# Kernel optimization log

Measured on AMD Instinct MI355X. Metric: run time of the kernel, lower is better.

The kernel has to match this reference:

```python
import jax, jax.numpy as jnp
import numpy as np

N_FFT = 1024
HOP = 256
CACHE = N_FFT - 1  # causal left padding
EPS = 1e-12
BATCH = 16
SAMPLES = HOP * 2048


def _make_weight():
    # DFT basis modulated by a periodic Hann window (torch.hann_window default).
    n = np.arange(N_FFT, dtype=np.float32)
    k = np.arange(N_FFT // 2 + 1, dtype=np.float32)[:, None]
    ang = (-2.0 * np.pi / N_FFT) * k * n[None, :]
    win = 0.5 * (1.0 - np.cos(2.0 * np.pi * n / N_FFT))
    w = np.concatenate([np.cos(ang), np.sin(ang)], axis=0) * win  # [2*(N//2+1), N_FFT]
    return jnp.asarray(w, dtype=jnp.float32)[:, None, :]  # [O, I=1, K]


def setup_inputs() -> dict:
    key = jax.random.key(0)
    x = jax.random.normal(key, (BATCH, SAMPLES), dtype=jnp.float32)
    return {"x": x, "weight": _make_weight()}


def reference(x, weight):
    if x.ndim == 2:
        x = x[:, None, :]  # [B, 1, T]
    # causal constant (zero) padding on the left
    x = jnp.pad(x, ((0, 0), (0, 0), (CACHE, 0)))
    # strided conv against the fixed DFT basis: [B, 2*(N//2+1), L]
    y = jax.lax.conv_general_dilated(
        x, weight, window_strides=(HOP,), padding='VALID',
        dimension_numbers=('NCH', 'OIH', 'NCH'))
    B, C, T = y.shape
    y = y.reshape(B, 2, C // 2, T)  # real/imag split
    mag = jnp.sqrt(jnp.clip(jnp.sum(y * y, axis=1), EPS, None))  # [B, N//2+1, L]
    return mag
```

## Files before the change

### kernel.cpp

```cpp
#include <hip/hip_runtime.h>
#include <stdint.h>

#define SAMPLES   524288
#define BATCH     16
#define T_FRAMES  2048
#define K_FFT     1024
#define HOPSZ     256
#define CACHEPAD  1023
#define NCH       513
#define XROW      525312

typedef __bf16          bf16x8 __attribute__((ext_vector_type(8)));
typedef float           f32x4  __attribute__((ext_vector_type(4)));
typedef unsigned short  u16x8  __attribute__((ext_vector_type(8)));

__device__ __forceinline__ unsigned short f2bf(float f) {
    union { float f; unsigned u; } v; v.f = f;
    unsigned r = v.u + 0x7fffu + ((v.u >> 16) & 1u);
    return (unsigned short)(r >> 16);
}

__global__ void prep(const float* __restrict__ x, const float* __restrict__ wsrc,
                     unsigned short* __restrict__ Xb, unsigned short* __restrict__ Wb) {
    const int bid = blockIdx.x;
    const int tid = threadIdx.x;
    if (bid < 512) {
        int gid = bid * 256 + tid;
        int m   = gid >> 7;
        int kc  = (gid & 127) << 3;
        int q = m >> 5, h = (m >> 4) & 1, r = m & 15;
        int bin  = q * 16 + r;
        int srow = (h == 0) ? bin : (bin == 0 ? 512 : NCH + bin);
        const float* s = wsrc + (long long)srow * K_FFT + kc;
        f32x4 a = *(const f32x4*)s;
        f32x4 c = *(const f32x4*)(s + 4);
        union { u16x8 v; unsigned short e[8]; } o;
        o.e[0]=f2bf(a[0]); o.e[1]=f2bf(a[1]); o.e[2]=f2bf(a[2]); o.e[3]=f2bf(a[3]);
        o.e[4]=f2bf(c[0]); o.e[5]=f2bf(c[1]); o.e[6]=f2bf(c[2]); o.e[7]=f2bf(c[3]);
        *(u16x8*)(Wb + (long long)m * K_FFT + kc) = o.v;
    } else {
        int id  = bid - 512;
        int bat = id >> 8;
        int bx  = id & 255;
        unsigned short* xbo = Xb + (long long)bat * XROW;
        if (bx == 0) {
            for (int j = tid; j < CACHEPAD; j += 256) xbo[j] = 0;
            if (tid == 0) xbo[XROW - 1] = 0;
        }
        int i0 = (bx * 256 + tid) * 8;
        const float* xb = x + (long long)bat * SAMPLES;
        f32x4 a = *(const f32x4*)&xb[i0];
        f32x4 c = *(const f32x4*)&xb[i0 + 4];
        unsigned short* dst = xbo + CACHEPAD + i0;
        dst[0]=f2bf(a[0]); dst[1]=f2bf(a[1]); dst[2]=f2bf(a[2]); dst[3]=f2bf(a[3]);
        dst[4]=f2bf(c[0]); dst[5]=f2bf(c[1]); dst[6]=f2bf(c[2]); dst[7]=f2bf(c[3]);
    }
}

__device__ __forceinline__ void gll16(const unsigned short* g, unsigned short* s) {
    __builtin_amdgcn_global_load_lds(
        (const __attribute__((address_space(1))) void*)g,
        (__attribute__((address_space(3))) void*)s,
        16, 0, 0);
}

__global__ __launch_bounds__(256, 3)
void stft_gemm(const unsigned short* __restrict__ Xb,
               const unsigned short* __restrict__ Wb,
               float* __restrict__ out) {
    __shared__ unsigned short Ws[128 * 64];
    __shared__ unsigned short Fs[128 * 64];

    const int id  = blockIdx.x;
    const int xcd = id & 7;
    const int idx = id >> 3;
    const int nt  = idx >> 5;
    const int ft  = (xcd << 5) | (idx & 31);

    const int tid = threadIdx.x;
    const int l   = tid & 63;
    const int w   = tid >> 6;
    const int ln  = l & 15;
    const int qd  = l >> 4;

    const int b  = ft >> 4;
    const int t0 = (ft & 15) * 128;

    const unsigned short* xbase = Xb + (long long)b * XROW;

    const int srow   = l >> 3;
    const int schunk = l & 7;

    const unsigned short* fsrc[4];
    const unsigned short* wsrc[4];
    unsigned short* fdst[4];
    unsigned short* wdst[4];
    #pragma unroll
    for (int c = 0; c < 4; ++c) {
        int r = w * 32 + c * 8 + srow;
        int gchunk = schunk ^ (r & 7);
        fsrc[c] = xbase + (t0 + r) * HOPSZ + gchunk * 8;
        wsrc[c] = Wb + ((long long)(nt * 128 + r)) * K_FFT + gchunk * 8;
        fdst[c] = Fs + (w * 32 + c * 8) * 64;
        wdst[c] = Ws + (w * 32 + c * 8) * 64;
    }

    const int wave_m = w & 1;
    const int wave_n = w >> 1;

    f32x4 acc[4][4];
    #pragma unroll
    for (int i = 0; i < 4; ++i)
        #pragma unroll
        for (int j = 0; j < 4; ++j)
            acc[i][j] = (f32x4){0.f, 0.f, 0.f, 0.f};

    int a_off[4][2], b_off[4][2];
    #pragma unroll
    for (int i = 0; i < 4; ++i)
        #pragma unroll
        for (int k2 = 0; k2 < 2; ++k2) {
            int ck = ((k2 * 4 + qd) ^ (ln & 7)) * 8;
            a_off[i][k2] = (wave_m * 64 + i * 16 + ln) * 64 + ck;
            b_off[i][k2] = (wave_n * 64 + i * 16 + ln) * 64 + ck;
        }

    for (int kk = 0; kk < K_FFT; kk += 64) {
        #pragma unroll
        for (int c = 0; c < 4; ++c) gll16(fsrc[c] + kk, fdst[c]);
        #pragma unroll
        for (int c = 0; c < 4; ++c) gll16(wsrc[c] + kk, wdst[c]);
        __syncthreads();

        #pragma unroll
        for (int k2 = 0; k2 < 2; ++k2) {
            bf16x8 av[4], bv[4];
            #pragma unroll
            for (int i = 0; i < 4; ++i) av[i] = *(const bf16x8*)&Ws[a_off[i][k2]];
            #pragma unroll
            for (int j = 0; j < 4; ++j) bv[j] = *(const bf16x8*)&Fs[b_off[j][k2]];
            #pragma unroll
            for (int i = 0; i < 4; ++i)
                #pragma unroll
                for (int j = 0; j < 4; ++j)
                    acc[i][j] = __builtin_amdgcn_mfma_f32_16x16x32_bf16(av[i], bv[j], acc[i][j], 0, 0, 0);
        }
        __syncthreads();
    }

    float* outb = out + (long long)b * (NCH * T_FRAMES);
    #pragma unroll
    for (int p = 0; p < 2; ++p) {
        #pragma unroll
        for (int j = 0; j < 4; ++j) {
            const int t = t0 + wave_n * 64 + j * 16 + ln;
            #pragma unroll
            for (int r = 0; r < 4; ++r) {
                float re  = acc[2 * p][j][r];
                float im  = acc[2 * p + 1][j][r];
                int bin = (nt * 4 + wave_m * 2 + p) * 16 + qd * 4 + r;
                if (bin == 0) {
                    outb[t] = sqrtf(fmaxf(re * re, 1e-12f));
                    outb[(long long)512 * T_FRAMES + t] = sqrtf(fmaxf(im * im, 1e-12f));
                } else {
                    outb[(long long)bin * T_FRAMES + t] =
                        sqrtf(fmaxf(re * re + im * im, 1e-12f));
                }
            }
        }
    }
}

extern "C" void kernel_launch(void* const* d_in, const int* in_sizes, int n_in,
                              void* d_out, int out_size, void* d_ws, size_t ws_size,
                              hipStream_t stream) {
    const float* x  = (const float*)d_in[0];
    const float* wt = (const float*)d_in[1];
    float* out = (float*)d_out;

    unsigned short* Xb = (unsigned short*)d_ws;
    unsigned short* Wb = (unsigned short*)((char*)d_ws + (size_t)33554432);

    prep<<<4608, 256, 0, stream>>>(x, wt, Xb, Wb);
    stft_gemm<<<2048, 256, 0, stream>>>(Xb, Wb, out);
}
```

Measured before the change: 154.1 us.

## Switch GEMM to 32x32x16 MFMA tiles and vectorize padded bf16 input stores

The inner product now uses 32x32x16 bf16 MFMA instructions with 2x2 accumulator tiles per wave instead of 4x4 tiles of 16x16x32. This cuts the number of MFMA issues and LDS fragment loads per k-step, and the epilogue is remapped so real and imaginary parts come from one accumulator. The prep kernel also shifts the bf16 input by one element so each thread writes an aligned 16-byte vector instead of eight scalar stores, patching the boundary element separately. The risk is correctness in the new accumulator-to-bin mapping and in the shifted padding layout.

```diff
diff --git a/kernel.cpp b/kernel.cpp
--- a/kernel.cpp
+++ b/kernel.cpp
@@ -12,6 +12,7 @@
 
 typedef __bf16          bf16x8 __attribute__((ext_vector_type(8)));
 typedef float           f32x4  __attribute__((ext_vector_type(4)));
+typedef float           f32x16 __attribute__((ext_vector_type(16)));
 typedef unsigned short  u16x8  __attribute__((ext_vector_type(8)));
 
 __device__ __forceinline__ unsigned short f2bf(float f) {
@@ -45,15 +46,18 @@
         unsigned short* xbo = Xb + (long long)bat * XROW;
         if (bx == 0) {
             for (int j = tid; j < CACHEPAD; j += 256) xbo[j] = 0;
-            if (tid == 0) xbo[XROW - 1] = 0;
         }
         int i0 = (bx * 256 + tid) * 8;
         const float* xb = x + (long long)bat * SAMPLES;
         f32x4 a = *(const f32x4*)&xb[i0];
         f32x4 c = *(const f32x4*)&xb[i0 + 4];
-        unsigned short* dst = xbo + CACHEPAD + i0;
-        dst[0]=f2bf(a[0]); dst[1]=f2bf(a[1]); dst[2]=f2bf(a[2]); dst[3]=f2bf(a[3]);
-        dst[4]=f2bf(c[0]); dst[5]=f2bf(c[1]); dst[6]=f2bf(c[2]); dst[7]=f2bf(c[3]);
+        float e = (i0 + 8 < SAMPLES) ? xb[i0 + 8] : 0.f;
+        union { u16x8 v; unsigned short s[8]; } o;
+        o.s[0]=f2bf(a[1]); o.s[1]=f2bf(a[2]); o.s[2]=f2bf(a[3]);
+        o.s[3]=f2bf(c[0]); o.s[4]=f2bf(c[1]); o.s[5]=f2bf(c[2]); o.s[6]=f2bf(c[3]);
+        o.s[7]=f2bf(e);
+        *(u16x8*)(xbo + 1024 + i0) = o.v;
+        if (i0 == 0) xbo[CACHEPAD] = f2bf(a[0]);
     }
 }
 
@@ -80,8 +84,6 @@
     const int tid = threadIdx.x;
     const int l   = tid & 63;
     const int w   = tid >> 6;
-    const int ln  = l & 15;
-    const int qd  = l >> 4;
 
     const int b  = ft >> 4;
     const int t0 = (ft & 15) * 128;
@@ -107,22 +109,25 @@
 
     const int wave_m = w & 1;
     const int wave_n = w >> 1;
+    const int l31 = l & 31;
+    const int lh  = l >> 5;
 
-    f32x4 acc[4][4];
+    f32x16 acc[2][2];
     #pragma unroll
-    for (int i = 0; i < 4; ++i)
+    for (int i = 0; i < 2; ++i)
         #pragma unroll
-        for (int j = 0; j < 4; ++j)
-            acc[i][j] = (f32x4){0.f, 0.f, 0.f, 0.f};
+        for (int j = 0; j < 2; ++j)
+            acc[i][j] = (f32x16){0.f,0.f,0.f,0.f,0.f,0.f,0.f,0.f,
+                                 0.f,0.f,0.f,0.f,0.f,0.f,0.f,0.f};
 
-    int a_off[4][2], b_off[4][2];
+    int a_off[2][4], b_off[2][4];
     #pragma unroll
-    for (int i = 0; i < 4; ++i)
+    for (int i = 0; i < 2; ++i)
         #pragma unroll
-        for (int k2 = 0; k2 < 2; ++k2) {
-            int ck = ((k2 * 4 + qd) ^ (ln & 7)) * 8;
-            a_off[i][k2] = (wave_m * 64 + i * 16 + ln) * 64 + ck;
-            b_off[i][k2] = (wave_n * 64 + i * 16 + ln) * 64 + ck;
+        for (int s = 0; s < 4; ++s) {
+            int ck = (((s * 2 + lh) ^ (l & 7))) * 8;
+            a_off[i][s] = (wave_m * 64 + i * 32 + l31) * 64 + ck;
+            b_off[i][s] = (wave_n * 64 + i * 32 + l31) * 64 + ck;
         }
 
     for (int kk = 0; kk < K_FFT; kk += 64) {
@@ -133,32 +138,32 @@
         __syncthreads();
 
         #pragma unroll
-        for (int k2 = 0; k2 < 2; ++k2) {
-            bf16x8 av[4], bv[4];
-            #pragma unroll
-            for (int i = 0; i < 4; ++i) av[i] = *(const bf16x8*)&Ws[a_off[i][k2]];
-            #pragma unroll
-            for (int j = 0; j < 4; ++j) bv[j] = *(const bf16x8*)&Fs[b_off[j][k2]];
-            #pragma unroll
-            for (int i = 0; i < 4; ++i)
-                #pragma unroll
-                for (int j = 0; j < 4; ++j)
-                    acc[i][j] = __builtin_amdgcn_mfma_f32_16x16x32_bf16(av[i], bv[j], acc[i][j], 0, 0, 0);
+        for (int s = 0; s < 4; ++s) {
+            bf16x8 a0 = *(const bf16x8*)&Ws[a_off[0][s]];
+            bf16x8 a1 = *(const bf16x8*)&Ws[a_off[1][s]];
+            bf16x8 b0 = *(const bf16x8*)&Fs[b_off[0][s]];
+            bf16x8 b1 = *(const bf16x8*)&Fs[b_off[1][s]];
+            acc[0][0] = __builtin_amdgcn_mfma_f32_32x32x16_bf16(a0, b0, acc[0][0], 0, 0, 0);
+            acc[0][1] = __builtin_amdgcn_mfma_f32_32x32x16_bf16(a0, b1, acc[0][1], 0, 0, 0);
+            acc[1][0] = __builtin_amdgcn_mfma_f32_32x32x16_bf16(a1, b0, acc[1][0], 0, 0, 0);
+            acc[1][1] = __builtin_amdgcn_mfma_f32_32x32x16_bf16(a1, b1, acc[1][1], 0, 0, 0);
         }
         __syncthreads();
     }
 
     float* outb = out + (long long)b * (NCH * T_FRAMES);
     #pragma unroll
-    for (int p = 0; p < 2; ++p) {
+    for (int i = 0; i < 2; ++i) {
+        const int group = nt * 4 + wave_m * 2 + i;
         #pragma unroll
-        for (int j = 0; j < 4; ++j) {
-            const int t = t0 + wave_n * 64 + j * 16 + ln;
+        for (int j = 0; j < 2; ++j) {
+            const int t = t0 + wave_n * 64 + j * 32 + l31;
             #pragma unroll
-            for (int r = 0; r < 4; ++r) {
-                float re  = acc[2 * p][j][r];
-                float im  = acc[2 * p + 1][j][r];
-                int bin = (nt * 4 + wave_m * 2 + p) * 16 + qd * 4 + r;
+            for (int r = 0; r < 8; ++r) {
+                const int mloc = (r & 3) + 8 * (r >> 2) + 4 * lh;
+                float re = acc[i][j][r];
+                float im = acc[i][j][r + 8];
+                int bin = group * 16 + mloc;
                 if (bin == 0) {
                     outb[t] = sqrtf(fmaxf(re * re, 1e-12f));
                     outb[(long long)512 * T_FRAMES + t] = sqrtf(fmaxf(im * im, 1e-12f));
```

Result: slower. 162.4 us (+5.4%).

## Exploit DFT symmetry to halve GEMM reduction via sum/difference frames

Applied to the files above, without the earlier changes.

Rewrites the STFT GEMM to use cosine/sine symmetry of the DFT basis. Each frame is folded into sum and difference halves (x[n]+x[N-n], x[n]-x[N-n]), so the real part uses only the sum frames and the imaginary part only the difference frames, over half the reduction length (512 instead of 1024). The prep kernel now materialises these folded frames explicitly, which is about twice the original signal footprint, and the work is split into two batch halves to bound workspace size. The intent is to halve MFMA work at the cost of a heavier preprocessing pass, more workspace traffic and four launches instead of two.

```diff
diff --git a/kernel.cpp b/kernel.cpp
--- a/kernel.cpp
+++ b/kernel.cpp
@@ -4,11 +4,14 @@
 #define SAMPLES   524288
 #define BATCH     16
 #define T_FRAMES  2048
-#define K_FFT     1024
 #define HOPSZ     256
-#define CACHEPAD  1023
 #define NCH       513
-#define XROW      525312
+#define KF        512
+#define MF        1152
+#define HALF_FR   16384
+
+#define SB_OFF    1183744
+#define DB_OFF    17960960
 
 typedef __bf16          bf16x8 __attribute__((ext_vector_type(8)));
 typedef float           f32x4  __attribute__((ext_vector_type(4)));
@@ -21,40 +24,67 @@
 }
 
 __global__ void prep(const float* __restrict__ x, const float* __restrict__ wsrc,
-                     unsigned short* __restrict__ Xb, unsigned short* __restrict__ Wb) {
-    const int bid = blockIdx.x;
+                     unsigned short* __restrict__ Wf,
+                     unsigned short* __restrict__ Sb,
+                     unsigned short* __restrict__ Db, int half) {
+    int bid = blockIdx.x;
     const int tid = threadIdx.x;
-    if (bid < 512) {
-        int gid = bid * 256 + tid;
-        int m   = gid >> 7;
-        int kc  = (gid & 127) << 3;
-        int q = m >> 5, h = (m >> 4) & 1, r = m & 15;
-        int bin  = q * 16 + r;
-        int srow = (h == 0) ? bin : (bin == 0 ? 512 : NCH + bin);
-        const float* s = wsrc + (long long)srow * K_FFT + kc;
-        f32x4 a = *(const f32x4*)s;
-        f32x4 c = *(const f32x4*)(s + 4);
-        union { u16x8 v; unsigned short e[8]; } o;
-        o.e[0]=f2bf(a[0]); o.e[1]=f2bf(a[1]); o.e[2]=f2bf(a[2]); o.e[3]=f2bf(a[3]);
-        o.e[4]=f2bf(c[0]); o.e[5]=f2bf(c[1]); o.e[6]=f2bf(c[2]); o.e[7]=f2bf(c[3]);
-        *(u16x8*)(Wb + (long long)m * K_FFT + kc) = o.v;
+    if (half == 0) {
+        if (bid < 288) {
+            int gid = bid * 256 + tid;
+            int m   = gid >> 6;
+            int n0  = (gid & 63) << 3;
+            int g = m >> 5, h = (m >> 4) & 1, r = m & 15;
+            int bin = g * 16 + r;
+            bool valid = h ? (bin >= 1 && bin <= 511) : (bin <= 512);
+            const float* ws = wsrc + (long long)(h ? NCH + bin : bin) * 1024;
+            union { u16x8 v; unsigned short e[8]; } o;
+            #pragma unroll
+            for (int e = 0; e < 8; ++e) {
+                int n = n0 + e;
+                float v = 0.f;
+                if (valid) v = (n < 511) ? ws[n + 1] : 0.5f * ws[512];
+                o.e[e] = f2bf(v);
+            }
+            *(u16x8*)(Wf + (long long)m * KF + n0) = o.v;
+            return;
+        }
+        bid -= 288;
+    }
+    const int fr = tid >> 6;
+    const int n0 = (tid & 63) << 3;
+    const long long f = (long long)bid * 4 + fr;
+    const int bat = half * 8 + (int)(f >> 11);
+    const int t   = (int)(f & 2047);
+    const float* xb = x + (long long)bat * SAMPLES;
+    float fwd[8], rev[8];
+    if (t >= 4) {
+        const f32x4* pf = (const f32x4*)(xb + (t * 256 + n0 - 1024));
+        f32x4 A = pf[0], B = pf[1], C = pf[2];
+        fwd[0]=A[2]; fwd[1]=A[3]; fwd[2]=B[0]; fwd[3]=B[1];
+        fwd[4]=B[2]; fwd[5]=B[3]; fwd[6]=C[0]; fwd[7]=C[1];
+        const f32x4* pr = (const f32x4*)(xb + (t * 256 - n0 - 8));
+        f32x4 D = pr[0], E = pr[1], F = pr[2];
+        rev[0]=F[0]; rev[1]=E[3]; rev[2]=E[2]; rev[3]=E[1];
+        rev[4]=E[0]; rev[5]=D[3]; rev[6]=D[2]; rev[7]=D[1];
     } else {
-        int id  = bid - 512;
-        int bat = id >> 8;
-        int bx  = id & 255;
-        unsigned short* xbo = Xb + (long long)bat * XROW;
-        if (bx == 0) {
-            for (int j = tid; j < CACHEPAD; j += 256) xbo[j] = 0;
-            if (tid == 0) xbo[XROW - 1] = 0;
-        }
-        int i0 = (bx * 256 + tid) * 8;
-        const float* xb = x + (long long)bat * SAMPLES;
-        f32x4 a = *(const f32x4*)&xb[i0];
-        f32x4 c = *(const f32x4*)&xb[i0 + 4];
-        unsigned short* dst = xbo + CACHEPAD + i0;
-        dst[0]=f2bf(a[0]); dst[1]=f2bf(a[1]); dst[2]=f2bf(a[2]); dst[3]=f2bf(a[3]);
-        dst[4]=f2bf(c[0]); dst[5]=f2bf(c[1]); dst[6]=f2bf(c[2]); dst[7]=f2bf(c[3]);
-    }
+        #pragma unroll
+        for (int e = 0; e < 8; ++e) {
+            int n  = n0 + e;
+            int pf = t * 256 + n + 1 - 1023;
+            int pr = t * 256 - n;
+            fwd[e] = (pf >= 0) ? xb[pf] : 0.f;
+            rev[e] = (pr >= 0) ? xb[pr] : 0.f;
+        }
+    }
+    union { u16x8 v; unsigned short e[8]; } so, dof;
+    #pragma unroll
+    for (int e = 0; e < 8; ++e) {
+        so.e[e]  = f2bf(fwd[e] + rev[e]);
+        dof.e[e] = f2bf(fwd[e] - rev[e]);
+    }
+    *(u16x8*)(Sb + f * KF + n0) = so.v;
+    *(u16x8*)(Db + f * KF + n0) = dof.v;
 }
 
 __device__ __forceinline__ void gll16(const unsigned short* g, unsigned short* s) {
@@ -65,17 +95,22 @@
 }
 
 __global__ __launch_bounds__(256, 3)
-void stft_gemm(const unsigned short* __restrict__ Xb,
-               const unsigned short* __restrict__ Wb,
-               float* __restrict__ out) {
+void stft_gemm(const unsigned short* __restrict__ Sb,
+               const unsigned short* __restrict__ Db,
+               const unsigned short* __restrict__ Wf,
+               float* __restrict__ out, int half) {
     __shared__ unsigned short Ws[128 * 64];
-    __shared__ unsigned short Fs[128 * 64];
+    __shared__ unsigned short Ss[128 * 64];
+    __shared__ unsigned short Ds[128 * 64];
 
     const int id  = blockIdx.x;
     const int xcd = id & 7;
     const int idx = id >> 3;
-    const int nt  = idx >> 5;
-    const int ft  = (xcd << 5) | (idx & 31);
+    const int nt  = idx >> 4;
+    const int ft  = (xcd << 4) | (idx & 15);
+    const int bh  = ft >> 4;
+    const int t0  = (ft & 15) * 128;
+    const long long fl0 = (long long)bh * 2048 + t0;
 
     const int tid = threadIdx.x;
     const int l   = tid & 63;
@@ -83,26 +118,25 @@
     const int ln  = l & 15;
     const int qd  = l >> 4;
 
-    const int b  = ft >> 4;
-    const int t0 = (ft & 15) * 128;
-
-    const unsigned short* xbase = Xb + (long long)b * XROW;
-
     const int srow   = l >> 3;
     const int schunk = l & 7;
 
-    const unsigned short* fsrc[4];
-    const unsigned short* wsrc[4];
-    unsigned short* fdst[4];
-    unsigned short* wdst[4];
+    const unsigned short* asrc[4];
+    const unsigned short* ssrc[4];
+    const unsigned short* dsrc[4];
+    unsigned short* adst[4];
+    unsigned short* sdst[4];
+    unsigned short* ddst[4];
     #pragma unroll
     for (int c = 0; c < 4; ++c) {
         int r = w * 32 + c * 8 + srow;
         int gchunk = schunk ^ (r & 7);
-        fsrc[c] = xbase + (t0 + r) * HOPSZ + gchunk * 8;
-        wsrc[c] = Wb + ((long long)(nt * 128 + r)) * K_FFT + gchunk * 8;
-        fdst[c] = Fs + (w * 32 + c * 8) * 64;
-        wdst[c] = Ws + (w * 32 + c * 8) * 64;
+        asrc[c] = Wf + (long long)(nt * 128 + r) * KF + gchunk * 8;
+        ssrc[c] = Sb + (fl0 + r) * KF + gchunk * 8;
+        dsrc[c] = Db + (fl0 + r) * KF + gchunk * 8;
+        adst[c] = Ws + (w * 32 + c * 8) * 64;
+        sdst[c] = Ss + (w * 32 + c * 8) * 64;
+        ddst[c] = Ds + (w * 32 + c * 8) * 64;
     }
 
     const int wave_m = w & 1;
@@ -125,29 +159,36 @@
             b_off[i][k2] = (wave_n * 64 + i * 16 + ln) * 64 + ck;
         }
 
-    for (int kk = 0; kk < K_FFT; kk += 64) {
-        #pragma unroll
-        for (int c = 0; c < 4; ++c) gll16(fsrc[c] + kk, fdst[c]);
-        #pragma unroll
-        for (int c = 0; c < 4; ++c) gll16(wsrc[c] + kk, wdst[c]);
+    for (int kk = 0; kk < KF; kk += 64) {
+        #pragma unroll
+        for (int c = 0; c < 4; ++c) gll16(asrc[c] + kk, adst[c]);
+        #pragma unroll
+        for (int c = 0; c < 4; ++c) gll16(ssrc[c] + kk, sdst[c]);
+        #pragma unroll
+        for (int c = 0; c < 4; ++c) gll16(dsrc[c] + kk, ddst[c]);
         __syncthreads();
 
         #pragma unroll
         for (int k2 = 0; k2 < 2; ++k2) {
-            bf16x8 av[4], bv[4];
+            bf16x8 av[4], bs[4], bd[4];
             #pragma unroll
             for (int i = 0; i < 4; ++i) av[i] = *(const bf16x8*)&Ws[a_off[i][k2]];
             #pragma unroll
-            for (int j = 0; j < 4; ++j) bv[j] = *(const bf16x8*)&Fs[b_off[j][k2]];
-            #pragma unroll
-            for (int i = 0; i < 4; ++i)
-                #pragma unroll
-                for (int j = 0; j < 4; ++j)
-                    acc[i][j] = __builtin_amdgcn_mfma_f32_16x16x32_bf16(av[i], bv[j], acc[i][j], 0, 0, 0);
+            for (int j = 0; j < 4; ++j) bs[j] = *(const bf16x8*)&Ss[b_off[j][k2]];
+            #pragma unroll
+            for (int j = 0; j < 4; ++j) bd[j] = *(const bf16x8*)&Ds[b_off[j][k2]];
+            #pragma unroll
+            for (int j = 0; j < 4; ++j) {
+                acc[0][j] = __builtin_amdgcn_mfma_f32_16x16x32_bf16(av[0], bs[j], acc[0][j], 0, 0, 0);
+                acc[1][j] = __builtin_amdgcn_mfma_f32_16x16x32_bf16(av[1], bd[j], acc[1][j], 0, 0, 0);
+                acc[2][j] = __builtin_amdgcn_mfma_f32_16x16x32_bf16(av[2], bs[j], acc[2][j], 0, 0, 0);
+                acc[3][j] = __builtin_amdgcn_mfma_f32_16x16x32_bf16(av[3], bd[j], acc[3][j], 0, 0, 0);
+            }
         }
         __syncthreads();
     }
 
+    const int b = half * 8 + bh;
     float* outb = out + (long long)b * (NCH * T_FRAMES);
     #pragma unroll
     for (int p = 0; p < 2; ++p) {
@@ -159,13 +200,9 @@
                 float re  = acc[2 * p][j][r];
                 float im  = acc[2 * p + 1][j][r];
                 int bin = (nt * 4 + wave_m * 2 + p) * 16 + qd * 4 + r;
-                if (bin == 0) {
-                    outb[t] = sqrtf(fmaxf(re * re, 1e-12f));
-                    outb[(long long)512 * T_FRAMES + t] = sqrtf(fmaxf(im * im, 1e-12f));
-                } else {
+                if (bin < NCH)
                     outb[(long long)bin * T_FRAMES + t] =
                         sqrtf(fmaxf(re * re + im * im, 1e-12f));
-                }
             }
         }
     }
@@ -178,9 +215,12 @@
     const float* wt = (const float*)d_in[1];
     float* out = (float*)d_out;
 
-    unsigned short* Xb = (unsigned short*)d_ws;
-    unsigned short* Wb = (unsigned short*)((char*)d_ws + (size_t)33554432);
-
-    prep<<<4608, 256, 0, stream>>>(x, wt, Xb, Wb);
-    stft_gemm<<<2048, 256, 0, stream>>>(Xb, Wb, out);
-}
+    unsigned short* Wf = (unsigned short*)d_ws;
+    unsigned short* Sb = (unsigned short*)((char*)d_ws + SB_OFF);
+    unsigned short* Db = (unsigned short*)((char*)d_ws + DB_OFF);
+
+    prep<<<4384, 256, 0, stream>>>(x, wt, Wf, Sb, Db, 0);
+    stft_gemm<<<1152, 256, 0, stream>>>(Sb, Db, Wf, out, 0);
+    prep<<<4096, 256, 0, stream>>>(x, wt, Wf, Sb, Db, 1);
+    stft_gemm<<<1152, 256, 0, stream>>>(Sb, Db, Wf, out, 1);
+}
```

Result: slower. 167.2 us (+8.5%).
